# Optimization experiments

Hardware: AMD Instinct MI355X
Metric: run time of the kernel (lower is better)

The kernel has to match this reference:

```python
import jax, jax.numpy as jnp
import numpy as np

H = W = 256
CX = CY = 128
N_RINGS = 16
RING_W = 8


def _ring_indices():
    """Static per-ring pixel coordinate lists (cv2 filled-circle rasterization
    approximated by Euclidean distance: ring i = { inner_r < dist <= outer_r }).
    Ring 0 excludes the exact center pixel, matching cv2.circle(radius=0) erase."""
    yy, xx = np.mgrid[0:H, 0:W]
    dist = np.sqrt((xx - CX) ** 2 + (yy - CY) ** 2)
    rings = []
    for i in range(N_RINGS):
        m = (dist <= (i + 1) * RING_W) & (dist > i * RING_W)
        ys, xs = np.nonzero(m)
        rings.append((jnp.asarray(ys), jnp.asarray(xs)))
    return rings

_RINGS = _ring_indices()


def setup_inputs() -> dict:
    key = jax.random.key(0)
    # normalized image in [0,1) so denorm->uint8 quantization never wraps
    image_tensor = jax.random.uniform(key, (256, 3, 256, 256), dtype=jnp.float32)
    return {"image_tensor": image_tensor}


def reference(image_tensor):
    # denormalize and quantize exactly like (img*0.5+0.5)*255 -> uint8 (truncation)
    img = jnp.floor((image_tensor * 0.5 + 0.5) * 255.0)  # [B,3,H,W], values 0..255
    feats = []
    for ys, xs in _RINGS:  # fixed 16-iteration structural loop
        px = img[:, :, ys, xs]                # [B, 3, N_ring] gather
        mean = jnp.mean(px, axis=-1)          # [B, 3]
        std = jnp.std(px, axis=-1)            # population std (ddof=0) like np
        med = jnp.median(px, axis=-1)         # [B, 3]
        feats.append(jnp.concatenate([mean, std, med], axis=-1))  # [B, 9]
    return jnp.stack(feats, axis=1)  # [B, 16, 9]
```

## Files before the change

kernel.cpp:

```cpp
#include <hip/hip_runtime.h>

#define IH 256
#define IW 256
#define NRINGS 16
#define HW_BRC 128

__global__ __launch_bounds__(1024)
void radial_fused(const float* __restrict__ img, float* __restrict__ out) {
    const int b   = blockIdx.x;
    const int tid = threadIdx.x;

    __shared__ unsigned int hist[NRINGS * 3 * HW_BRC];

    for (int i = tid; i < NRINGS * 3 * HW_BRC; i += 1024) hist[i] = 0u;
    __syncthreads();

    const int xg = (tid & 63) * 4;
    const int r0 = tid >> 6;
    const float* base = img + (size_t)b * 3 * IH * IW;

    const int dx0 = xg - 128;
    int dxs[4];
    #pragma unroll
    for (int j = 0; j < 4; ++j) dxs[j] = (dx0 + j) * (dx0 + j);
    const int admin  = (dx0 <= 0 && dx0 + 3 >= 0) ? 0 : min(abs(dx0), abs(dx0 + 3));
    const int admin2 = admin * admin;

    for (int k = 0; k < 16; ++k) {
        const int y   = r0 + (k << 4);
        const int dy  = y - 128;
        const int dy2 = dy * dy;
        if (dy2 + admin2 > 16384) continue;

        const int off = y * IW + xg;
        const float4 f0 = *(const float4*)(base + off);
        const float4 f1 = *(const float4*)(base + IH * IW + off);
        const float4 f2 = *(const float4*)(base + 2 * IH * IW + off);
        const float va[3][4] = {{f0.x, f0.y, f0.z, f0.w},
                                {f1.x, f1.y, f1.z, f1.w},
                                {f2.x, f2.y, f2.z, f2.w}};

        #pragma unroll
        for (int j = 0; j < 4; ++j) {
            const int d2 = dy2 + dxs[j];
            if (d2 == 0 || d2 > 16384) continue;
            int kk = (int)ceilf(sqrtf((float)d2) * 0.125f);
            if (64 * kk * kk < d2) kk++;
            else if (kk > 1 && 64 * (kk - 1) * (kk - 1) >= d2) kk--;
            const int ring = kk - 1;
            #pragma unroll
            for (int c = 0; c < 3; ++c) {
                const float f = va[c][j];
                int iv = (int)floorf((f * 0.5f + 0.5f) * 255.0f);
                iv = min(max(iv, 0), 255);
                atomicAdd(&hist[(ring * 3 + c) * HW_BRC + (iv >> 1)],
                          1u << ((iv & 1) << 4));
            }
        }
    }

    __syncthreads();

    if (tid < NRINGS * 3) {
        const int ring = tid / 3;
        const int c    = tid - ring * 3;
        const unsigned int* h = &hist[(ring * 3 + c) * HW_BRC];

        unsigned int n = 0, sum = 0, sumsq = 0;
        #pragma unroll 8
        for (int w = 0; w < HW_BRC; ++w) {
            const unsigned int v  = h[w];
            const unsigned int c0 = v & 0xffffu;
            const unsigned int c1 = v >> 16;
            const unsigned int v0 = 2 * w, v1 = 2 * w + 1;
            n     += c0 + c1;
            sum   += c0 * v0 + c1 * v1;
            sumsq += c0 * v0 * v0 + c1 * v1 * v1;
        }

        const double dn   = (double)n;
        const double mean = (double)sum / dn;
        double var = (double)sumsq / dn - mean * mean;
        if (var < 0.0) var = 0.0;

        const unsigned int j1 = (n - 1u) >> 1;
        const unsigned int j2 = n >> 1;
        unsigned int cum = 0;
        int v1i = -1, v2i = -1;
        for (int w = 0; w < HW_BRC; ++w) {
            const unsigned int v = h[w];
            cum += v & 0xffffu;
            if (v1i < 0 && cum > j1) v1i = 2 * w;
            if (v2i < 0 && cum > j2) { v2i = 2 * w; break; }
            cum += v >> 16;
            if (v1i < 0 && cum > j1) v1i = 2 * w + 1;
            if (v2i < 0 && cum > j2) { v2i = 2 * w + 1; break; }
        }

        float* o = out + ((size_t)b * NRINGS + ring) * 9;
        o[c]     = (float)mean;
        o[3 + c] = (float)sqrt(var);
        o[6 + c] = 0.5f * (float)(v1i + v2i);
    }
}

extern "C" void kernel_launch(void* const* d_in, const int* in_sizes, int n_in,
                              void* d_out, int out_size, void* d_ws, size_t ws_size,
                              hipStream_t stream) {
    const float* img = (const float*)d_in[0];
    float* out = (float*)d_out;
    radial_fused<<<256, 1024, 0, stream>>>(img, out);
}
```

Measured before the change: 284.9 us.

## Precompute ring-index LUT in a prelaunch kernel and use full 256-bin histograms

```diff
diff --git a/kernel.cpp b/kernel.cpp
--- a/kernel.cpp
+++ b/kernel.cpp
@@ -3,35 +3,61 @@
 #define IH 256
 #define IW 256
 #define NRINGS 16
-#define HW_BRC 128
+#define LUT_WORDS (IH * IW / 4)
+
+__global__ __launch_bounds__(256)
+void k_ringlut(unsigned int* __restrict__ lut) {
+    const int gid = blockIdx.x * 256 + threadIdx.x;
+    const int y   = gid >> 6;
+    const int x0  = (gid & 63) * 4;
+    const int dy  = y - 128;
+    const int dy2 = dy * dy;
+    unsigned int w = 0;
+    #pragma unroll
+    for (int j = 0; j < 4; ++j) {
+        const int dx = x0 + j - 128;
+        const int d2 = dy2 + dx * dx;
+        unsigned int r;
+        if (d2 == 0 || d2 > 16384) r = 255u;
+        else {
+            int kk = (int)ceilf(sqrtf((float)d2) * 0.125f);
+            if (64 * kk * kk < d2) kk++;
+            else if (kk > 1 && 64 * (kk - 1) * (kk - 1) >= d2) kk--;
+            r = (unsigned)(kk - 1);
+        }
+        w |= r << (8 * j);
+    }
+    lut[gid] = w;
+}
 
 __global__ __launch_bounds__(1024)
-void radial_fused(const float* __restrict__ img, float* __restrict__ out) {
+void radial_fused(const float* __restrict__ img,
+                  const unsigned int* __restrict__ lut,
+                  float* __restrict__ out) {
     const int b   = blockIdx.x;
     const int tid = threadIdx.x;
 
-    __shared__ unsigned int hist[NRINGS * 3 * HW_BRC];
+    __shared__ unsigned int hist[NRINGS * 3 * 256];
 
-    for (int i = tid; i < NRINGS * 3 * HW_BRC; i += 1024) hist[i] = 0u;
+    for (int i = tid; i < NRINGS * 3 * 256; i += 1024) hist[i] = 0u;
     __syncthreads();
 
     const int xg = (tid & 63) * 4;
     const int r0 = tid >> 6;
     const float* base = img + (size_t)b * 3 * IH * IW;
+    const int lc = xg >> 2;
 
-    const int dx0 = xg - 128;
-    int dxs[4];
+    unsigned int rw[16];
     #pragma unroll
-    for (int j = 0; j < 4; ++j) dxs[j] = (dx0 + j) * (dx0 + j);
-    const int admin  = (dx0 <= 0 && dx0 + 3 >= 0) ? 0 : min(abs(dx0), abs(dx0 + 3));
-    const int admin2 = admin * admin;
+    for (int k = 0; k < 16; ++k) {
+        const int y = r0 + (k << 4);
+        rw[k] = lut[(y << 6) + lc];
+    }
 
+    #pragma unroll
     for (int k = 0; k < 16; ++k) {
+        if (rw[k] == 0xFFFFFFFFu) continue;
         const int y   = r0 + (k << 4);
-        const int dy  = y - 128;
-        const int dy2 = dy * dy;
-        if (dy2 + admin2 > 16384) continue;
-
         const int off = y * IW + xg;
         const float4 f0 = *(const float4*)(base + off);
         const float4 f1 = *(const float4*)(base + IH * IW + off);
@@ -42,19 +68,14 @@
 
         #pragma unroll
         for (int j = 0; j < 4; ++j) {
-            const int d2 = dy2 + dxs[j];
-            if (d2 == 0 || d2 > 16384) continue;
-            int kk = (int)ceilf(sqrtf((float)d2) * 0.125f);
-            if (64 * kk * kk < d2) kk++;
-            else if (kk > 1 && 64 * (kk - 1) * (kk - 1) >= d2) kk--;
-            const int ring = kk - 1;
+            const unsigned int ring = (rw[k] >> (8 * j)) & 255u;
+            if (ring == 255u) continue;
+            unsigned int* hb = &hist[(ring * 3) << 8];
             #pragma unroll
             for (int c = 0; c < 3; ++c) {
                 const float f = va[c][j];
-                int iv = (int)floorf((f * 0.5f + 0.5f) * 255.0f);
-                iv = min(max(iv, 0), 255);
-                atomicAdd(&hist[(ring * 3 + c) * HW_BRC + (iv >> 1)],
-                          1u << ((iv & 1) << 4));
+                const int iv = (int)floorf((f * 0.5f + 0.5f) * 255.0f);
+                atomicAdd(&hb[(c << 8) + iv], 1u);
             }
         }
     }
@@ -64,18 +85,15 @@
     if (tid < NRINGS * 3) {
         const int ring = tid / 3;
         const int c    = tid - ring * 3;
-        const unsigned int* h = &hist[(ring * 3 + c) * HW_BRC];
+        const unsigned int* h = &hist[((ring * 3 + c) << 8)];
 
         unsigned int n = 0, sum = 0, sumsq = 0;
         #pragma unroll 8
-        for (int w = 0; w < HW_BRC; ++w) {
-            const unsigned int v  = h[w];
-            const unsigned int c0 = v & 0xffffu;
-            const unsigned int c1 = v >> 16;
-            const unsigned int v0 = 2 * w, v1 = 2 * w + 1;
-            n     += c0 + c1;
-            sum   += c0 * v0 + c1 * v1;
-            sumsq += c0 * v0 * v0 + c1 * v1 * v1;
+        for (int v = 0; v < 256; ++v) {
+            const unsigned int cnt = h[v];
+            n     += cnt;
+            sum   += cnt * (unsigned)v;
+            sumsq += cnt * (unsigned)(v * v);
         }
 
         const double dn   = (double)n;
@@ -87,14 +105,10 @@
         const unsigned int j2 = n >> 1;
         unsigned int cum = 0;
         int v1i = -1, v2i = -1;
-        for (int w = 0; w < HW_BRC; ++w) {
-            const unsigned int v = h[w];
-            cum += v & 0xffffu;
-            if (v1i < 0 && cum > j1) v1i = 2 * w;
-            if (v2i < 0 && cum > j2) { v2i = 2 * w; break; }
-            cum += v >> 16;
-            if (v1i < 0 && cum > j1) v1i = 2 * w + 1;
-            if (v2i < 0 && cum > j2) { v2i = 2 * w + 1; break; }
+        for (int v = 0; v < 256; ++v) {
+            cum += h[v];
+            if (v1i < 0 && cum > j1) v1i = v;
+            if (cum > j2) { v2i = v; break; }
         }
 
         float* o = out + ((size_t)b * NRINGS + ring) * 9;
@@ -109,5 +123,7 @@
                               hipStream_t stream) {
     const float* img = (const float*)d_in[0];
     float* out = (float*)d_out;
-    radial_fused<<<256, 1024, 0, stream>>>(img, out);
+    unsigned int* lut = (unsigned int*)d_ws;
+    k_ringlut<<<LUT_WORDS / 256, 256, 0, stream>>>(lut);
+    radial_fused<<<256, 1024, 0, stream>>>(img, lut, out);
 }
```

Result: no change. 288.0 us (+1.1%).
